# Performance work log

Hardware: AMD Instinct MI355X
Metric: run time of the kernel (lower is better)

## Reference

```python
import jax, jax.numpy as jnp
import numpy as np

S, B, D, H, L = 1000, 4, 1024, 16, 4
HD = D // H
FF = 4 * D
V = 64
OUT = 64


def setup_inputs() -> dict:
    key = jax.random.key(0)
    ks = jax.random.split(key, 10)
    w = lambda k, shape: jax.random.normal(k, shape, jnp.float32) * 0.02
    return {
        'tokens': jax.random.randint(ks[0], (S, B), 0, V),
        'embed': w(ks[1], (V, D)),
        'Wq': w(ks[2], (L, D, D)), 'bq': jnp.zeros((L, D), jnp.float32),
        'Wk': w(ks[3], (L, D, D)), 'bk': jnp.zeros((L, D), jnp.float32),
        'Wv': w(ks[4], (L, D, D)), 'bv': jnp.zeros((L, D), jnp.float32),
        'Wo': w(ks[5], (L, D, D)), 'bo': jnp.zeros((L, D), jnp.float32),
        'ln1_g': jnp.ones((L, D), jnp.float32), 'ln1_b': jnp.zeros((L, D), jnp.float32),
        'ln2_g': jnp.ones((L, D), jnp.float32), 'ln2_b': jnp.zeros((L, D), jnp.float32),
        'W1': w(ks[6], (L, FF, D)), 'b1': jnp.zeros((L, FF), jnp.float32),
        'W2': w(ks[7], (L, D, FF)), 'b2': jnp.zeros((L, D), jnp.float32),
        'Wout': w(ks[8], (OUT, D)), 'bout': jnp.zeros((OUT,), jnp.float32),
    }


def _ln(x, g, b):
    m = x.mean(-1, keepdims=True)
    v = ((x - m) ** 2).mean(-1, keepdims=True)
    return (x - m) * jax.lax.rsqrt(v + 1e-5) * g + b


def _rope(x):
    # x: [B, H, S, HD]; matches RotaryEmbedding: x*cos + rotate_half(x)*sin
    hd = x.shape[-1]
    inv_freq = 1.0 / (10000.0 ** (jnp.arange(0, hd, 2, dtype=jnp.float32) / hd))
    t = jnp.arange(x.shape[2], dtype=jnp.float32)
    freqs = t[:, None] * inv_freq[None, :]          # [S, HD/2]
    emb = jnp.concatenate([freqs, freqs], -1)       # [S, HD]
    cos, sin = jnp.cos(emb), jnp.sin(emb)
    x1, x2 = jnp.split(x, 2, -1)
    rot = jnp.concatenate([-x2, x1], -1)
    return x * cos + rot * sin


def _attn(x, Wq, bq, Wk, bk, Wv, bv, Wo, bo):
    # x: [S, B, D]; manual rotary MHA path (eval: no dropout, masks None)
    s, b, d = x.shape
    scale = HD ** -0.5
    q = (jnp.einsum('sbd,ed->sbe', x, Wq) + bq) * scale
    k = jnp.einsum('sbd,ed->sbe', x, Wk) + bk
    v = jnp.einsum('sbd,ed->sbe', x, Wv) + bv
    split = lambda t: t.reshape(s, b, H, HD).transpose(1, 2, 0, 3)  # [B,H,S,HD]
    q, k, v = split(q), split(k), split(v)
    q, k = _rope(q), _rope(k)
    scores = jnp.einsum('bhsd,bhtd->bhst', q, k)
    p = jax.nn.softmax(scores, axis=-1)
    o = jnp.einsum('bhst,bhtd->bhsd', p, v)
    o = o.transpose(2, 0, 1, 3).reshape(s, b, d)
    return jnp.einsum('sbd,ed->sbe', o, Wo) + bo


def reference(tokens, embed, Wq, bq, Wk, bk, Wv, bv, Wo, bo,
              ln1_g, ln1_b, ln2_g, ln2_b, W1, b1, W2, b2, Wout, bout):
    x = embed[tokens]  # [S, B, D]
    for i in range(L):
        h = _ln(x, ln1_g[i], ln1_b[i])
        x = x + _attn(h, Wq[i], bq[i], Wk[i], bk[i], Wv[i], bv[i], Wo[i], bo[i])
        h = _ln(x, ln2_g[i], ln2_b[i])
        h = jax.nn.gelu(jnp.einsum('sbd,fd->sbf', h, W1[i]) + b1[i], approximate=False)
        x = x + jnp.einsum('sbf,df->sbd', h, W2[i]) + b2[i]
    return jnp.einsum('sbd,od->sbo', x, Wout) + bout
```

## Files before the change

### kernel.cpp

```cpp
#include <hip/hip_runtime.h>
#include <hip/hip_bf16.h>
#include <math.h>

#define S_   1000
#define B_   4
#define D_   1024
#define H_   16
#define HD_  64
#define L_   4
#define FF_  4096
#define N_   (S_*B_)

typedef __bf16 bf16x8 __attribute__((ext_vector_type(8)));
typedef float  f32x4  __attribute__((ext_vector_type(4)));
typedef __attribute__((address_space(3))) unsigned short lds_u16;

__device__ __forceinline__ unsigned short f2b(float f) {
    unsigned u = __builtin_bit_cast(unsigned, f);
    u = (u + 0x7FFFu + ((u >> 16) & 1u)) >> 16;
    return (unsigned short)u;
}
__device__ __forceinline__ float b2f(unsigned short s) {
    unsigned u = (unsigned)s << 16;
    return __builtin_bit_cast(float, u);
}

__device__ __forceinline__ void gl16(const void* g, void* l) {
    __builtin_amdgcn_global_load_lds(
        (const __attribute__((address_space(1))) unsigned int*)g,
        (__attribute__((address_space(3))) unsigned int*)l, 16, 0, 0);
}

__device__ __forceinline__ bf16x8 ldsr(unsigned addr) {
    bf16x8 r;
    asm volatile("ds_read_b128 %0, %1" : "=v"(r) : "v"(addr));
    return r;
}

__global__ void embed_kernel(const int* __restrict__ tokens,
                             const float* __restrict__ emb,
                             float* __restrict__ x) {
    int n = blockIdx.x;
    int tok = tokens[n];
    const float4* src = (const float4*)(emb + (size_t)tok * D_);
    float4* dst = (float4*)(x + (size_t)n * D_);
    dst[threadIdx.x] = src[threadIdx.x];
}

__global__ __launch_bounds__(256)
void cvtw_kernel(const float* __restrict__ wq, const float* __restrict__ wk,
                 const float* __restrict__ wv, const float* __restrict__ wo,
                 const float* __restrict__ w1, const float* __restrict__ w2,
                 unsigned short* __restrict__ dst) {
    const size_t M1 = (size_t)D_ * D_;
    const size_t M4 = (size_t)FF_ * D_;
    size_t i = ((size_t)blockIdx.x * 256 + threadIdx.x) * 4;
    const float* src; size_t off;
    if      (i < M1)        { src = wq; off = i; }
    else if (i < 2*M1)      { src = wk; off = i - M1; }
    else if (i < 3*M1)      { src = wv; off = i - 2*M1; }
    else if (i < 4*M1)      { src = wo; off = i - 3*M1; }
    else if (i < 4*M1+M4)   { src = w1; off = i - 4*M1; }
    else                    { src = w2; off = i - 4*M1 - M4; }
    float4 v = *(const float4*)(src + off);
    ushort4 u;
    u.x = f2b(v.x); u.y = f2b(v.y); u.z = f2b(v.z); u.w = f2b(v.w);
    *(ushort4*)(dst + i) = u;
}

__global__ __launch_bounds__(256)
void ln_kernel(const float* __restrict__ in,
               const float* __restrict__ g,
               const float* __restrict__ b,
               unsigned short* __restrict__ out) {
    int n = blockIdx.x;
    int tid = threadIdx.x;
    const float4* row = (const float4*)(in + (size_t)n * D_);
    float4 v = row[tid];
    float s  = v.x + v.y + v.z + v.w;
    float sq = v.x*v.x + v.y*v.y + v.z*v.z + v.w*v.w;
    #pragma unroll
    for (int off = 32; off; off >>= 1) {
        s  += __shfl_down(s, off);
        sq += __shfl_down(sq, off);
    }
    __shared__ float rs[4], rq[4];
    int wid = tid >> 6;
    if ((tid & 63) == 0) { rs[wid] = s; rq[wid] = sq; }
    __syncthreads();
    s  = rs[0] + rs[1] + rs[2] + rs[3];
    sq = rq[0] + rq[1] + rq[2] + rq[3];
    float mean = s * (1.0f / D_);
    float var  = sq * (1.0f / D_) - mean * mean;
    float rstd = rsqrtf(var + 1e-5f);
    float4 gg = ((const float4*)g)[tid];
    float4 bb = ((const float4*)b)[tid];
    ushort4 o;
    o.x = f2b((v.x - mean) * rstd * gg.x + bb.x);
    o.y = f2b((v.y - mean) * rstd * gg.y + bb.y);
    o.z = f2b((v.z - mean) * rstd * gg.z + bb.z);
    o.w = f2b((v.w - mean) * rstd * gg.w + bb.w);
    ((ushort4*)(out + (size_t)n * D_))[tid] = o;
}

template<int MODE>
__global__ __launch_bounds__(256, 2)
void agemm_kernel(const unsigned short* __restrict__ A,
                  const unsigned short* __restrict__ W,
                  const float* __restrict__ bb0, const float* __restrict__ bb1,
                  const float* __restrict__ bb2,
                  const float* __restrict__ res,
                  void* __restrict__ o0v, unsigned short* __restrict__ o1,
                  unsigned short* __restrict__ o2,
                  int M, int K) {
    __shared__ __align__(16) unsigned short As[2][128 * 64];
    __shared__ __align__(16) unsigned short Bs[2][128 * 64];
    int tid = threadIdx.x;
    int w = tid >> 6, lane = tid & 63;
    int wr = w >> 1, wc = w & 1;
    int m0 = blockIdx.x * 128, e0 = blockIdx.y * 128;
    int l15 = lane & 15, l4 = lane >> 4, l7 = lane & 7;

    f32x4 acc[4][4] = {};

    auto stage = [&](int buf, int kt) {
        #pragma unroll
        for (int rep = 0; rep < 4; ++rep) {
            int slot = rep * 256 + tid;
            int r = slot >> 3, c = slot & 7;
            int ar = m0 + r; if (ar > M - 1) ar = M - 1;
            gl16(A + (size_t)ar * K + kt + (c ^ (r & 7)) * 8, &As[buf][slot * 8]);
        }
        #pragma unroll
        for (int rep = 0; rep < 4; ++rep) {
            int slot = rep * 256 + tid;
            int r = slot >> 3, c = slot & 7;
            gl16(W + (size_t)(e0 + r) * K + kt + (c ^ (r & 7)) * 8, &Bs[buf][slot * 8]);
        }
    };

    int aoff[4], boff[4];
    #pragma unroll
    for (int i = 0; i < 4; ++i) {
        aoff[i] = (wr * 64 + i * 16 + l15) * 128;
        boff[i] = (wc * 64 + i * 16 + l15) * 128;
    }

    stage(0, 0);
    asm volatile("s_waitcnt vmcnt(0)" ::: "memory");
    __builtin_amdgcn_sched_barrier(0);
    __builtin_amdgcn_s_barrier();

    int nk = K >> 6;
    for (int t = 0; t < nk; ++t) {
        int cur = t & 1;
        if (t + 1 < nk) stage(cur ^ 1, (t + 1) << 6);
        __builtin_amdgcn_sched_barrier(0);
        unsigned aB = (unsigned)(size_t)(lds_u16*)&As[cur][0];
        unsigned bB = (unsigned)(size_t)(lds_u16*)&Bs[cur][0];
        #pragma unroll
        for (int ks = 0; ks < 2; ++ks) {
            unsigned soff = (unsigned)((((ks * 4) + l4) ^ l7) * 16);
            bf16x8 av[4], bv[4];
            #pragma unroll
            for (int i = 0; i < 4; ++i) av[i] = ldsr(aB + aoff[i] + soff);
            #pragma unroll
            for (int j = 0; j < 4; ++j) bv[j] = ldsr(bB + boff[j] + soff);
            asm volatile("s_waitcnt lgkmcnt(0)" ::: "memory");
            __builtin_amdgcn_sched_barrier(0);
            __builtin_amdgcn_s_setprio(1);
            #pragma unroll
            for (int i = 0; i < 4; ++i)
                #pragma unroll
                for (int j = 0; j < 4; ++j)
                    acc[i][j] = __builtin_amdgcn_mfma_f32_16x16x32_bf16(av[i], bv[j], acc[i][j], 0, 0, 0);
            __builtin_amdgcn_s_setprio(0);
        }
        asm volatile("s_waitcnt vmcnt(0)" ::: "memory");
        __builtin_amdgcn_sched_barrier(0);
        __builtin_amdgcn_s_barrier();
    }

    if (MODE == 0) {
        int sel = e0 >> 10;
        int eobase = (e0 & 1023) + wc * 64;
        const float* bp = (sel == 0) ? bb0 : (sel == 1) ? bb1 : bb2;
        unsigned short* op = (sel == 0) ? (unsigned short*)o0v : (sel == 1) ? o1 : o2;
        float scale = (sel == 0) ? 0.125f : 1.0f;
        #pragma unroll
        for (int i = 0; i < 4; ++i) {
            int mrow = m0 + wr*64 + i*16 + l4*4;
            #pragma unroll
            for (int j = 0; j < 4; ++j) {
                int eo = eobase + j*16 + l15;
                float bval = bp[eo];
                #pragma unroll
                for (int r = 0; r < 4; ++r) {
                    int m = mrow + r;
                    if (m >= M) continue;
                    op[(size_t)m * 1024 + eo] = f2b((acc[i][j][r] + bval) * scale);
                }
            }
        }
    } else if (MODE == 1) {
        unsigned short* op = (unsigned short*)o0v;
        #pragma unroll
        for (int i = 0; i < 4; ++i) {
            int mrow = m0 + wr*64 + i*16 + l4*4;
            #pragma unroll
            for (int j = 0; j < 4; ++j) {
                int e = e0 + wc*64 + j*16 + l15;
                float bval = bb0[e];
                #pragma unroll
                for (int r = 0; r < 4; ++r) {
                    int m = mrow + r;
                    if (m >= M) continue;
                    float val = acc[i][j][r] + bval;
                    val = 0.5f * val * (1.0f + erff(val * 0.70710678118654752f));
                    op[(size_t)m * FF_ + e] = f2b(val);
                }
            }
        }
    } else {
        float* op = (float*)o0v;
        #pragma unroll
        for (int i = 0; i < 4; ++i) {
            int mrow = m0 + wr*64 + i*16 + l4*4;
            #pragma unroll
            for (int j = 0; j < 4; ++j) {
                int e = e0 + wc*64 + j*16 + l15;
                float bval = bb0[e];
                #pragma unroll
                for (int r = 0; r < 4; ++r) {
                    int m = mrow + r;
                    if (m >= M) continue;
                    float val = acc[i][j][r] + bval + res[(size_t)m * 1024 + e];
                    op[(size_t)m * 1024 + e] = val;
                }
            }
        }
    }
}

__global__ __launch_bounds__(256)
void gemm_kernel(const float* __restrict__ A, const float* __restrict__ W,
                 const float* __restrict__ bias, float* __restrict__ C,
                 int M, int K, int E) {
    __shared__ float As[32][64];
    __shared__ float Ws[32][64];
    int tid = threadIdx.x;
    int m0 = blockIdx.x * 64, e0 = blockIdx.y * 64;
    int tx = tid & 15, ty = tid >> 4;
    int lrow = tid >> 2;
    int lkc  = (tid & 3) * 8;
    float acc[4][4] = {};
    const float* Arow = A + (size_t)(m0 + lrow) * K + lkc;
    const float* Wrow = W + (size_t)(e0 + lrow) * K + lkc;
    bool aval = (m0 + lrow) < M;

    for (int k0 = 0; k0 < K; k0 += 32) {
        float4 a0 = make_float4(0.f,0.f,0.f,0.f), a1 = a0;
        if (aval) {
            a0 = *(const float4*)(Arow + k0);
            a1 = *(const float4*)(Arow + k0 + 4);
        }
        float4 w0 = *(const float4*)(Wrow + k0);
        float4 w1 = *(const float4*)(Wrow + k0 + 4);
        As[lkc+0][lrow] = a0.x; As[lkc+1][lrow] = a0.y;
        As[lkc+2][lrow] = a0.z; As[lkc+3][lrow] = a0.w;
        As[lkc+4][lrow] = a1.x; As[lkc+5][lrow] = a1.y;
        As[lkc+6][lrow] = a1.z; As[lkc+7][lrow] = a1.w;
        Ws[lkc+0][lrow] = w0.x; Ws[lkc+1][lrow] = w0.y;
        Ws[lkc+2][lrow] = w0.z; Ws[lkc+3][lrow] = w0.w;
        Ws[lkc+4][lrow] = w1.x; Ws[lkc+5][lrow] = w1.y;
        Ws[lkc+6][lrow] = w1.z; Ws[lkc+7][lrow] = w1.w;
        __syncthreads();
        #pragma unroll
        for (int kk = 0; kk < 32; ++kk) {
            float4 a = *(const float4*)(&As[kk][ty*4]);
            float4 ww = *(const float4*)(&Ws[kk][tx*4]);
            acc[0][0] += a.x*ww.x; acc[0][1] += a.x*ww.y; acc[0][2] += a.x*ww.z; acc[0][3] += a.x*ww.w;
            acc[1][0] += a.y*ww.x; acc[1][1] += a.y*ww.y; acc[1][2] += a.y*ww.z; acc[1][3] += a.y*ww.w;
            acc[2][0] += a.z*ww.x; acc[2][1] += a.z*ww.y; acc[2][2] += a.z*ww.z; acc[2][3] += a.z*ww.w;
            acc[3][0] += a.w*ww.x; acc[3][1] += a.w*ww.y; acc[3][2] += a.w*ww.z; acc[3][3] += a.w*ww.w;
        }
        __syncthreads();
    }
    #pragma unroll
    for (int i = 0; i < 4; ++i) {
        int m = m0 + ty*4 + i;
        if (m >= M) continue;
        #pragma unroll
        for (int j = 0; j < 4; ++j) {
            int e = e0 + tx*4 + j;
            C[(size_t)m * E + e] = acc[i][j] + bias[e];
        }
    }
}

__global__ void ropeb_kernel(unsigned short* __restrict__ x) {
    int idx = blockIdx.x * 256 + threadIdx.x;
    if (idx >= N_ * H_ * 32) return;
    int j = idx & 31;
    int h = (idx >> 5) & (H_ - 1);
    int n = idx >> 9;
    int s = n >> 2;
    float inv = __expf(-(float)j * 0.2878231366242557f);
    float ang = (float)s * inv;
    float sn, cs;
    __sincosf(ang, &sn, &cs);
    unsigned short* p = x + (size_t)n * D_ + h * HD_ + j;
    float a = b2f(p[0]), c = b2f(p[32]);
    p[0]  = f2b(a * cs - c * sn);
    p[32] = f2b(c * cs + a * sn);
}

__global__ __launch_bounds__(256)
void vtr_kernel(const unsigned short* __restrict__ vin,
                unsigned short* __restrict__ vout) {
    __shared__ unsigned short T[64][65];
    int tt = blockIdx.x;
    int bh = blockIdx.y;
    int b = bh >> 4, h = bh & 15;
    int tid = threadIdx.x;
    #pragma unroll
    for (int rep = 0; rep < 2; ++rep) {
        int slot = rep * 256 + tid;
        int r = slot >> 3, ch = slot & 7;
        int t = tt * 64 + r;
        unsigned short e[8] = {0,0,0,0,0,0,0,0};
        if (t < S_) {
            const unsigned short* src = vin + ((size_t)t * B_ + b) * D_ + h * HD_ + ch * 8;
            *(ushort4*)&e[0] = *(const ushort4*)(src);
            *(ushort4*)&e[4] = *(const ushort4*)(src + 4);
        }
        #pragma unroll
        for (int u = 0; u < 8; ++u) T[r][ch*8+u] = e[u];
    }
    __syncthreads();
    #pragma unroll
    for (int rep = 0; rep < 2; ++rep) {
        int slot = rep * 256 + tid;
        int d = slot >> 3, ch = slot & 7;
        unsigned short e[8];
        #pragma unroll
        for (int u = 0; u < 8; ++u) e[u] = T[ch*8+u][d];
        unsigned short* dst = vout + ((size_t)bh * 64 + d) * 1024 + tt * 64 + ch * 8;
        *(ushort4*)(dst)     = *(ushort4*)&e[0];
        *(ushort4*)(dst + 4) = *(ushort4*)&e[4];
    }
}

__global__ __launch_bounds__(256)
void mattn_kernel(const unsigned short* __restrict__ qg,
                  const unsigned short* __restrict__ kg,
                  const unsigned short* __restrict__ vt,
                  unsigned short* __restrict__ o) {
    __shared__ __align__(16) unsigned short Ks[64 * 64];
    __shared__ __align__(16) unsigned short Vs[64 * 64];
    __shared__ __align__(16) unsigned short Ps[4][16 * 64];

    int bid = blockIdx.x;
    int qt = bid & 15;
    int bh = bid >> 4;
    int b = bh >> 4, h = bh & 15;
    int tid = threadIdx.x;
    int w = tid >> 6, lane = tid & 63;
    int l15 = lane & 15, l4 = lane >> 4, l7 = lane & 7;
    int q0 = qt * 64 + w * 16;

    int srow = lane >> 3;
    int schunk = ((lane & 7) ^ srow) * 8;

    bf16x8 qfr[2];
    {
        int qr = q0 + l15; if (qr > S_ - 1) qr = S_ - 1;
        const unsigned short* qrow = qg + ((size_t)qr * B_ + b) * D_ + h * HD_;
        qfr[0] = *(const bf16x8*)(qrow + l4 * 8);
        qfr[1] = *(const bf16x8*)(qrow + 32 + l4 * 8);
    }

    f32x4 accO[4] = {};
    float mreg[4] = {-1e30f, -1e30f, -1e30f, -1e30f};
    float lreg[4] = {0.f, 0.f, 0.f, 0.f};

    for (int t0 = 0; t0 < 1024; t0 += 64) {
        __syncthreads();
        #pragma unroll
        for (int c = 0; c < 2; ++c) {
            int r0 = w * 16 + c * 8;
            int tr = t0 + r0 + srow; if (tr > S_ - 1) tr = S_ - 1;
            gl16(kg + ((size_t)tr * B_ + b) * D_ + h * HD_ + schunk, &Ks[r0 * 64]);
            gl16(vt + ((size_t)bh * 64 + r0 + srow) * 1024 + t0 + schunk, &Vs[r0 * 64]);
        }
        __syncthreads();

        f32x4 s[4] = {};
        #pragma unroll
        for (int ks = 0; ks < 2; ++ks) {
            int cc = ks * 4 + l4;
            int slot = (cc ^ l7) * 16;
            #pragma unroll
            for (int j = 0; j < 4; ++j) {
                bf16x8 kf = *(const bf16x8*)((const char*)Ks + (j*16 + l15) * 128 + slot);
                s[j] = __builtin_amdgcn_mfma_f32_16x16x32_bf16(qfr[ks], kf, s[j], 0, 0, 0);
            }
        }
        #pragma unroll
        for (int j = 0; j < 4; ++j) {
            int t = t0 + j * 16 + l15;
            if (t >= S_) { s[j][0] = -1e30f; s[j][1] = -1e30f; s[j][2] = -1e30f; s[j][3] = -1e30f; }
        }
        float rm[4], sc[4], rsum[4];
        #pragma unroll
        for (int r = 0; r < 4; ++r)
            rm[r] = fmaxf(fmaxf(s[0][r], s[1][r]), fmaxf(s[2][r], s[3][r]));
        #pragma unroll
        for (int mk = 1; mk <= 8; mk <<= 1) {
            #pragma unroll
            for (int r = 0; r < 4; ++r) rm[r] = fmaxf(rm[r], __shfl_xor(rm[r], mk));
        }
        #pragma unroll
        for (int r = 0; r < 4; ++r) {
            float mn = fmaxf(mreg[r], rm[r]);
            sc[r] = __expf(mreg[r] - mn);
            mreg[r] = mn;
            rsum[r] = 0.f;
        }
        #pragma unroll
        for (int j = 0; j < 4; ++j) {
            int inb = (j * 16 + l15) * 2;
            #pragma unroll
            for (int r = 0; r < 4; ++r) {
                float p = __expf(s[j][r] - mreg[r]);
                rsum[r] += p;
                int row = l4 * 4 + r;
                *(unsigned short*)((char*)&Ps[w][0] + row * 128 +
                    ((((inb >> 4) ^ (row & 7)) << 4)) + (inb & 15)) = f2b(p);
            }
        }
        #pragma unroll
        for (int mk = 1; mk <= 8; mk <<= 1) {
            #pragma unroll
            for (int r = 0; r < 4; ++r) rsum[r] += __shfl_xor(rsum[r], mk);
        }
        #pragma unroll
        for (int r = 0; r < 4; ++r) lreg[r] = lreg[r] * sc[r] + rsum[r];
        #pragma unroll
        for (int j = 0; j < 4; ++j) {
            accO[j][0] *= sc[0]; accO[j][1] *= sc[1];
            accO[j][2] *= sc[2]; accO[j][3] *= sc[3];
        }
        #pragma unroll
        for (int ks = 0; ks < 2; ++ks) {
            int cc = ks * 4 + l4;
            int slot = (cc ^ l7) * 16;
            bf16x8 pf = *(const bf16x8*)((const char*)&Ps[w][0] + l15 * 128 + slot);
            #pragma unroll
            for (int j = 0; j < 4; ++j) {
                bf16x8 vf = *(const bf16x8*)((const char*)Vs + (j*16 + l15) * 128 + slot);
                accO[j] = __builtin_amdgcn_mfma_f32_16x16x32_bf16(pf, vf, accO[j], 0, 0, 0);
            }
        }
    }
    #pragma unroll
    for (int r = 0; r < 4; ++r) {
        int q = q0 + l4 * 4 + r;
        if (q >= S_) continue;
        float inv = 1.0f / lreg[r];
        unsigned short* orow = o + ((size_t)q * B_ + b) * D_ + h * HD_;
        #pragma unroll
        for (int j = 0; j < 4; ++j)
            orow[j * 16 + l15] = f2b(accO[j][r] * inv);
    }
}

extern "C" void kernel_launch(void* const* d_in, const int* in_sizes, int n_in,
                              void* d_out, int out_size, void* d_ws, size_t ws_size,
                              hipStream_t stream) {
    const int*   tokens = (const int*)  d_in[0];
    const float* Wemb   = (const float*)d_in[1];
    const float* Wq     = (const float*)d_in[2];
    const float* bq     = (const float*)d_in[3];
    const float* Wk     = (const float*)d_in[4];
    const float* bk     = (const float*)d_in[5];
    const float* Wv     = (const float*)d_in[6];
    const float* bv     = (const float*)d_in[7];
    const float* Wo     = (const float*)d_in[8];
    const float* bo     = (const float*)d_in[9];
    const float* ln1g   = (const float*)d_in[10];
    const float* ln1b   = (const float*)d_in[11];
    const float* ln2g   = (const float*)d_in[12];
    const float* ln2b   = (const float*)d_in[13];
    const float* W1     = (const float*)d_in[14];
    const float* b1     = (const float*)d_in[15];
    const float* W2     = (const float*)d_in[16];
    const float* b2     = (const float*)d_in[17];
    const float* Wout   = (const float*)d_in[18];
    const float* bout   = (const float*)d_in[19];
    float* out = (float*)d_out;

    const size_t ND = (size_t)N_ * D_;
    const size_t NF = (size_t)N_ * FF_;
    const size_t M1 = (size_t)D_ * D_;
    const size_t M4 = (size_t)FF_ * D_;
    const size_t VT = (size_t)64 * 64 * 1024;

    float* x  = (float*)d_ws;
    unsigned short* hb = (unsigned short*)(x + ND);
    unsigned short* qb = hb + ND;
    unsigned short* kb = qb + ND;
    unsigned short* vb = kb + ND;
    unsigned short* ob = vb + ND;
    unsigned short* vt = ob + ND;
    unsigned short* f1 = vt + VT;
    unsigned short* wb = f1 + NF;

    dim3 blk(256);
    embed_kernel<<<N_, blk, 0, stream>>>(tokens, Wemb, x);

    dim3 gQKV(32, 24);
    dim3 gW1(32, 32);
    dim3 gE(32, 8);
    dim3 gCv(12288);
    int rth = N_ * H_ * 32;
    dim3 gR((rth + 255) / 256);
    dim3 gVt(16, 64);
    dim3 gAt(16 * 64);
    dim3 gOut((N_ + 63) / 64, 1);

    for (int l = 0; l < L_; ++l) {
        cvtw_kernel<<<gCv, blk, 0, stream>>>(Wq + l*M1, Wk + l*M1, Wv + l*M1,
                                             Wo + l*M1, W1 + l*M4, W2 + l*M4, wb);
        ln_kernel<<<N_, blk, 0, stream>>>(x, ln1g + l*D_, ln1b + l*D_, hb);
        agemm_kernel<0><<<gQKV, blk, 0, stream>>>(hb, wb,
            bq + l*D_, bk + l*D_, bv + l*D_, nullptr, qb, kb, vb, N_, D_);
        ropeb_kernel<<<gR, blk, 0, stream>>>(qb);
        ropeb_kernel<<<gR, blk, 0, stream>>>(kb);
        vtr_kernel<<<gVt, blk, 0, stream>>>(vb, vt);
        mattn_kernel<<<gAt, blk, 0, stream>>>(qb, kb, vt, ob);
        agemm_kernel<2><<<gE, blk, 0, stream>>>(ob, wb + 3*M1,
            bo + l*D_, nullptr, nullptr, x, x, nullptr, nullptr, N_, D_);
        ln_kernel<<<N_, blk, 0, stream>>>(x, ln2g + l*D_, ln2b + l*D_, hb);
        agemm_kernel<1><<<gW1, blk, 0, stream>>>(hb, wb + 4*M1,
            b1 + l*FF_, nullptr, nullptr, nullptr, f1, nullptr, nullptr, N_, D_);
        agemm_kernel<2><<<gE, blk, 0, stream>>>(f1, wb + 4*M1 + M4,
            b2 + l*D_, nullptr, nullptr, x, x, nullptr, nullptr, N_, FF_);
    }
    gemm_kernel<<<gOut, blk, 0, stream>>>(x, Wout, bout, out, N_, D_, 64);
}
```

Baseline: 1.269 ms.

## Shrink GEMM tiles to 64x64 with triple-buffered loads and fuse RoPE into QKV epilogue

```diff
diff --git a/kernel.cpp b/kernel.cpp
--- a/kernel.cpp
+++ b/kernel.cpp
@@ -104,8 +104,8 @@
 }
 
 template<int MODE>
-__global__ __launch_bounds__(256, 2)
-void agemm_kernel(const unsigned short* __restrict__ A,
+__global__ __launch_bounds__(256, 3)
+void rgemm_kernel(const unsigned short* __restrict__ A,
                   const unsigned short* __restrict__ W,
                   const float* __restrict__ bb0, const float* __restrict__ bb1,
                   const float* __restrict__ bb2,
@@ -113,109 +113,137 @@
                   void* __restrict__ o0v, unsigned short* __restrict__ o1,
                   unsigned short* __restrict__ o2,
                   int M, int K) {
-    __shared__ __align__(16) unsigned short As[2][128 * 64];
-    __shared__ __align__(16) unsigned short Bs[2][128 * 64];
+    __shared__ __align__(16) unsigned short As[3][64 * 64];
+    __shared__ __align__(16) unsigned short Bs[3][64 * 64];
     int tid = threadIdx.x;
     int w = tid >> 6, lane = tid & 63;
     int wr = w >> 1, wc = w & 1;
-    int m0 = blockIdx.x * 128, e0 = blockIdx.y * 128;
+    int m0 = blockIdx.x * 64, e0 = blockIdx.y * 64;
     int l15 = lane & 15, l4 = lane >> 4, l7 = lane & 7;
 
-    f32x4 acc[4][4] = {};
-
-    auto stage = [&](int buf, int kt) {
-        #pragma unroll
-        for (int rep = 0; rep < 4; ++rep) {
+    f32x4 acc[2][2] = {};
+
+    auto stage = [&](int rs, int kt) {
+        #pragma unroll
+        for (int rep = 0; rep < 2; ++rep) {
             int slot = rep * 256 + tid;
             int r = slot >> 3, c = slot & 7;
             int ar = m0 + r; if (ar > M - 1) ar = M - 1;
-            gl16(A + (size_t)ar * K + kt + (c ^ (r & 7)) * 8, &As[buf][slot * 8]);
-        }
-        #pragma unroll
-        for (int rep = 0; rep < 4; ++rep) {
+            gl16(A + (size_t)ar * K + kt + (c ^ (r & 7)) * 8, &As[rs][slot * 8]);
+        }
+        #pragma unroll
+        for (int rep = 0; rep < 2; ++rep) {
             int slot = rep * 256 + tid;
             int r = slot >> 3, c = slot & 7;
-            gl16(W + (size_t)(e0 + r) * K + kt + (c ^ (r & 7)) * 8, &Bs[buf][slot * 8]);
+            gl16(W + (size_t)(e0 + r) * K + kt + (c ^ (r & 7)) * 8, &Bs[rs][slot * 8]);
         }
     };
 
-    int aoff[4], boff[4];
-    #pragma unroll
-    for (int i = 0; i < 4; ++i) {
-        aoff[i] = (wr * 64 + i * 16 + l15) * 128;
-        boff[i] = (wc * 64 + i * 16 + l15) * 128;
-    }
-
+    int aoff[2], boff[2];
+    #pragma unroll
+    for (int i = 0; i < 2; ++i)  aoff[i]  = (wr * 32 + i * 16 + l15) * 128;
+    #pragma unroll
+    for (int jj = 0; jj < 2; ++jj) boff[jj] = (wc * 16 + jj * 32 + l15) * 128;
+
+    int nk = K >> 6;
     stage(0, 0);
-    asm volatile("s_waitcnt vmcnt(0)" ::: "memory");
-    __builtin_amdgcn_sched_barrier(0);
-    __builtin_amdgcn_s_barrier();
-
-    int nk = K >> 6;
+    if (nk > 1) stage(1, 64);
     for (int t = 0; t < nk; ++t) {
-        int cur = t & 1;
-        if (t + 1 < nk) stage(cur ^ 1, (t + 1) << 6);
+        int rs = t % 3;
+        if (t + 2 < nk) {
+            stage((t + 2) % 3, (t + 2) << 6);
+            asm volatile("s_waitcnt vmcnt(8)" ::: "memory");
+        } else if (t + 1 < nk) {
+            asm volatile("s_waitcnt vmcnt(4)" ::: "memory");
+        } else {
+            asm volatile("s_waitcnt vmcnt(0)" ::: "memory");
+        }
         __builtin_amdgcn_sched_barrier(0);
-        unsigned aB = (unsigned)(size_t)(lds_u16*)&As[cur][0];
-        unsigned bB = (unsigned)(size_t)(lds_u16*)&Bs[cur][0];
+        __builtin_amdgcn_s_barrier();
+        unsigned aB = (unsigned)(size_t)(lds_u16*)&As[rs][0];
+        unsigned bB = (unsigned)(size_t)(lds_u16*)&Bs[rs][0];
         #pragma unroll
         for (int ks = 0; ks < 2; ++ks) {
             unsigned soff = (unsigned)((((ks * 4) + l4) ^ l7) * 16);
-            bf16x8 av[4], bv[4];
-            #pragma unroll
-            for (int i = 0; i < 4; ++i) av[i] = ldsr(aB + aoff[i] + soff);
-            #pragma unroll
-            for (int j = 0; j < 4; ++j) bv[j] = ldsr(bB + boff[j] + soff);
+            bf16x8 av[2], bv[2];
+            #pragma unroll
+            for (int i = 0; i < 2; ++i)  av[i]  = ldsr(aB + aoff[i] + soff);
+            #pragma unroll
+            for (int jj = 0; jj < 2; ++jj) bv[jj] = ldsr(bB + boff[jj] + soff);
             asm volatile("s_waitcnt lgkmcnt(0)" ::: "memory");
             __builtin_amdgcn_sched_barrier(0);
             __builtin_amdgcn_s_setprio(1);
             #pragma unroll
-            for (int i = 0; i < 4; ++i)
+            for (int i = 0; i < 2; ++i)
                 #pragma unroll
-                for (int j = 0; j < 4; ++j)
-                    acc[i][j] = __builtin_amdgcn_mfma_f32_16x16x32_bf16(av[i], bv[j], acc[i][j], 0, 0, 0);
+                for (int jj = 0; jj < 2; ++jj)
+                    acc[i][jj] = __builtin_amdgcn_mfma_f32_16x16x32_bf16(av[i], bv[jj], acc[i][jj], 0, 0, 0);
             __builtin_amdgcn_s_setprio(0);
         }
-        asm volatile("s_waitcnt vmcnt(0)" ::: "memory");
         __builtin_amdgcn_sched_barrier(0);
         __builtin_amdgcn_s_barrier();
     }
 
     if (MODE == 0) {
         int sel = e0 >> 10;
-        int eobase = (e0 & 1023) + wc * 64;
+        int eobase = e0 & 1023;
         const float* bp = (sel == 0) ? bb0 : (sel == 1) ? bb1 : bb2;
         unsigned short* op = (sel == 0) ? (unsigned short*)o0v : (sel == 1) ? o1 : o2;
-        float scale = (sel == 0) ? 0.125f : 1.0f;
-        #pragma unroll
-        for (int i = 0; i < 4; ++i) {
-            int mrow = m0 + wr*64 + i*16 + l4*4;
-            #pragma unroll
-            for (int j = 0; j < 4; ++j) {
-                int eo = eobase + j*16 + l15;
-                float bval = bp[eo];
+        if (sel == 2) {
+            #pragma unroll
+            for (int i = 0; i < 2; ++i) {
+                int mrow = m0 + wr*32 + i*16 + l4*4;
+                #pragma unroll
+                for (int jj = 0; jj < 2; ++jj) {
+                    int eo = eobase + wc*16 + jj*32 + l15;
+                    float bval = bp[eo];
+                    #pragma unroll
+                    for (int r = 0; r < 4; ++r) {
+                        int m = mrow + r;
+                        if (m >= M) continue;
+                        op[(size_t)m * 1024 + eo] = f2b(acc[i][jj][r] + bval);
+                    }
+                }
+            }
+        } else {
+            float scale = (sel == 0) ? 0.125f : 1.0f;
+            #pragma unroll
+            for (int i = 0; i < 2; ++i) {
+                int mrow = m0 + wr*32 + i*16 + l4*4;
+                int d5 = wc*16 + l15;
+                int eo_a = eobase + d5;
+                int eo_b = eo_a + 32;
+                float ba = bp[eo_a], bbv = bp[eo_b];
+                float invf = __expf(-(float)d5 * 0.2878231366242557f);
                 #pragma unroll
                 for (int r = 0; r < 4; ++r) {
                     int m = mrow + r;
                     if (m >= M) continue;
-                    op[(size_t)m * 1024 + eo] = f2b((acc[i][j][r] + bval) * scale);
+                    int s = m >> 2;
+                    float ang = (float)s * invf;
+                    float sn, cs;
+                    __sincosf(ang, &sn, &cs);
+                    float a = acc[i][0][r] + ba;
+                    float c = acc[i][1][r] + bbv;
+                    op[(size_t)m * 1024 + eo_a] = f2b((a*cs - c*sn) * scale);
+                    op[(size_t)m * 1024 + eo_b] = f2b((c*cs + a*sn) * scale);
                 }
             }
         }
     } else if (MODE == 1) {
         unsigned short* op = (unsigned short*)o0v;
         #pragma unroll
-        for (int i = 0; i < 4; ++i) {
-            int mrow = m0 + wr*64 + i*16 + l4*4;
-            #pragma unroll
-            for (int j = 0; j < 4; ++j) {
-                int e = e0 + wc*64 + j*16 + l15;
+        for (int i = 0; i < 2; ++i) {
+            int mrow = m0 + wr*32 + i*16 + l4*4;
+            #pragma unroll
+            for (int jj = 0; jj < 2; ++jj) {
+                int e = e0 + wc*16 + jj*32 + l15;
                 float bval = bb0[e];
                 #pragma unroll
                 for (int r = 0; r < 4; ++r) {
                     int m = mrow + r;
                     if (m >= M) continue;
-                    float val = acc[i][j][r] + bval;
+                    float val = acc[i][jj][r] + bval;
                     val = 0.5f * val * (1.0f + erff(val * 0.70710678118654752f));
                     op[(size_t)m * FF_ + e] = f2b(val);
                 }
@@ -224,18 +252,17 @@
     } else {
         float* op = (float*)o0v;
         #pragma unroll
-        for (int i = 0; i < 4; ++i) {
-            int mrow = m0 + wr*64 + i*16 + l4*4;
-            #pragma unroll
-            for (int j = 0; j < 4; ++j) {
-                int e = e0 + wc*64 + j*16 + l15;
+        for (int i = 0; i < 2; ++i) {
+            int mrow = m0 + wr*32 + i*16 + l4*4;
+            #pragma unroll
+            for (int jj = 0; jj < 2; ++jj) {
+                int e = e0 + wc*16 + jj*32 + l15;
                 float bval = bb0[e];
                 #pragma unroll
                 for (int r = 0; r < 4; ++r) {
                     int m = mrow + r;
                     if (m >= M) continue;
-                    float val = acc[i][j][r] + bval + res[(size_t)m * 1024 + e];
-                    op[(size_t)m * 1024 + e] = val;
+                    op[(size_t)m * 1024 + e] = acc[i][jj][r] + bval + res[(size_t)m * 1024 + e];
                 }
             }
         }
@@ -296,23 +323,6 @@
             C[(size_t)m * E + e] = acc[i][j] + bias[e];
         }
     }
-}
-
-__global__ void ropeb_kernel(unsigned short* __restrict__ x) {
-    int idx = blockIdx.x * 256 + threadIdx.x;
-    if (idx >= N_ * H_ * 32) return;
-    int j = idx & 31;
-    int h = (idx >> 5) & (H_ - 1);
-    int n = idx >> 9;
-    int s = n >> 2;
-    float inv = __expf(-(float)j * 0.2878231366242557f);
-    float ang = (float)s * inv;
-    float sn, cs;
-    __sincosf(ang, &sn, &cs);
-    unsigned short* p = x + (size_t)n * D_ + h * HD_ + j;
-    float a = b2f(p[0]), c = b2f(p[32]);
-    p[0]  = f2b(a * cs - c * sn);
-    p[32] = f2b(c * cs + a * sn);
 }
 
 __global__ __launch_bounds__(256)
@@ -519,12 +529,10 @@
     dim3 blk(256);
     embed_kernel<<<N_, blk, 0, stream>>>(tokens, Wemb, x);
 
-    dim3 gQKV(32, 24);
-    dim3 gW1(32, 32);
-    dim3 gE(32, 8);
+    dim3 gQKV(63, 48);
+    dim3 gW1(63, 64);
+    dim3 gE64(63, 16);
     dim3 gCv(12288);
-    int rth = N_ * H_ * 32;
-    dim3 gR((rth + 255) / 256);
     dim3 gVt(16, 64);
     dim3 gAt(16 * 64);
     dim3 gOut((N_ + 63) / 64, 1);
@@ -533,18 +541,16 @@
         cvtw_kernel<<<gCv, blk, 0, stream>>>(Wq + l*M1, Wk + l*M1, Wv + l*M1,
                                              Wo + l*M1, W1 + l*M4, W2 + l*M4, wb);
         ln_kernel<<<N_, blk, 0, stream>>>(x, ln1g + l*D_, ln1b + l*D_, hb);
-        agemm_kernel<0><<<gQKV, blk, 0, stream>>>(hb, wb,
+        rgemm_kernel<0><<<gQKV, blk, 0, stream>>>(hb, wb,
             bq + l*D_, bk + l*D_, bv + l*D_, nullptr, qb, kb, vb, N_, D_);
-        ropeb_kernel<<<gR, blk, 0, stream>>>(qb);
-        ropeb_kernel<<<gR, blk, 0, stream>>>(kb);
         vtr_kernel<<<gVt, blk, 0, stream>>>(vb, vt);
         mattn_kernel<<<gAt, blk, 0, stream>>>(qb, kb, vt, ob);
-        agemm_kernel<2><<<gE, blk, 0, stream>>>(ob, wb + 3*M1,
+        rgemm_kernel<2><<<gE64, blk, 0, stream>>>(ob, wb + 3*M1,
             bo + l*D_, nullptr, nullptr, x, x, nullptr, nullptr, N_, D_);
         ln_kernel<<<N_, blk, 0, stream>>>(x, ln2g + l*D_, ln2b + l*D_, hb);
-        agemm_kernel<1><<<gW1, blk, 0, stream>>>(hb, wb + 4*M1,
+        rgemm_kernel<1><<<gW1, blk, 0, stream>>>(hb, wb + 4*M1,
             b1 + l*FF_, nullptr, nullptr, nullptr, f1, nullptr, nullptr, N_, D_);
-        agemm_kernel<2><<<gE, blk, 0, stream>>>(f1, wb + 4*M1 + M4,
+        rgemm_kernel<2><<<gE64, blk, 0, stream>>>(f1, wb + 4*M1 + M4,
             b2 + l*D_, nullptr, nullptr, x, x, nullptr, nullptr, N_, FF_);
     }
     gemm_kernel<<<gOut, blk, 0, stream>>>(x, Wout, bout, out, N_, D_, 64);
```

Result: slower. 1.551 ms (+22.2%).
